# Performance work log

Hardware: AMD Instinct MI355X
Metric: run time of the kernel (lower is better)

## Reference

```python
import jax, jax.numpy as jnp
import numpy as np

T, N, F, H = 64, 20000, 8, 32
E = 320000
NEG_SLOPE = 0.01  # torch.nn.LeakyReLU default


def setup_inputs() -> dict:
    key = jax.random.key(0)
    ks = jax.random.split(key, 16)
    g = lambda k, shape, fan_in: jax.random.normal(k, shape, jnp.float32) * (1.0 / np.sqrt(fan_in))
    return {
        "x": jax.random.normal(ks[0], (T, N, F), jnp.float32),
        "edge_index": jax.random.randint(ks[1], (2, E), 0, N, jnp.int64),
        "edge_weight": jax.random.uniform(ks[2], (E,), jnp.float32),
        "h": jnp.zeros((N, H), jnp.float32),
        # GConvGRU(K=1): each ChebConv reduces to a dense Linear (only T_0 = X term)
        "Wxz": g(ks[3], (F, H), F), "bxz": jnp.zeros((H,), jnp.float32),
        "Whz": g(ks[4], (H, H), H), "bhz": jnp.zeros((H,), jnp.float32),
        "Wxr": g(ks[5], (F, H), F), "bxr": jnp.zeros((H,), jnp.float32),
        "Whr": g(ks[6], (H, H), H), "bhr": jnp.zeros((H,), jnp.float32),
        "Wxh": g(ks[7], (F, H), F), "bxh": jnp.zeros((H,), jnp.float32),
        "Whh": g(ks[8], (H, H), H), "bhh": jnp.zeros((H,), jnp.float32),
        "W1": g(ks[9], (H, 1), H), "b1": jnp.zeros((1,), jnp.float32),
        "W2": g(ks[10], (N, 1), N), "b2": jnp.zeros((1,), jnp.float32),
    }


def reference(x, edge_index, edge_weight, h,
              Wxz, bxz, Whz, bhz, Wxr, bxr, Whr, bhr, Wxh, bxh, Whh, bhh,
              W1, b1, W2, b2):
    # GConvGRU with Chebyshev order K=1: each ChebConv is out = X @ W + b
    # (edge_index / edge_weight only participate for K >= 2, faithful to source).
    def gru_step(hc, xt):  # hc: [N,H], xt: [N,F]
        z = jax.nn.sigmoid(xt @ Wxz + bxz + hc @ Whz + bhz)
        r = jax.nn.sigmoid(xt @ Wxr + bxr + hc @ Whr + bhr)
        h_tilde = jnp.tanh(xt @ Wxh + bxh + (hc * r) @ Whh + bhh)
        hn = z * hc + (1.0 - z) * h_tilde
        return hn, hn

    h_fin, h_tensor = jax.lax.scan(gru_step, h, x)  # h_tensor: [T,N,H]
    a = jax.nn.leaky_relu(h_tensor, NEG_SLOPE)       # LeakyReLU(h_tensor)
    a = jax.nn.leaky_relu(a @ W1 + b1, NEG_SLOPE)    # linear1 -> [T,N,1], then LeakyReLU
    a = a[..., 0]                                    # squeeze -> [T,N]
    out = (a @ W2 + b2)[..., 0]                      # linear2 -> [T,1] -> squeeze -> [T]
    return (out, h_fin)
```

## Files before the change

### kernel.cpp

```cpp
#include <hip/hip_runtime.h>

#define T_STEPS 64
#define N_NODES 20000
#define F_IN    8
#define H_DIM   32
#define NEG_SLOPE 0.01f
#define WS_STRIDE 32
#define LOG2E 1.44269504f

typedef __attribute__((ext_vector_type(8))) short bf16x8;
typedef __attribute__((ext_vector_type(4))) float f32x4;

#define MFMA(a, b, c) __builtin_amdgcn_mfma_f32_16x16x32_bf16((a), (b), (c), 0, 0, 0)

__device__ __forceinline__ unsigned short f2bf(float f) {
    unsigned u = __float_as_uint(f);
    u += 0x7FFFu + ((u >> 16) & 1u);
    return (unsigned short)(u >> 16);
}
__device__ __forceinline__ float bf2f(unsigned short s) {
    return __uint_as_float(((unsigned)s) << 16);
}
__device__ __forceinline__ void split_pack8_rne(const float* v, bf16x8& hi, bf16x8& lo) {
    union { unsigned u[4]; bf16x8 v8; } H, L;
#pragma unroll
    for (int p = 0; p < 4; ++p) {
        float a = v[2*p], b = v[2*p+1];
        unsigned short ha = f2bf(a), hb = f2bf(b);
        unsigned short la = f2bf(a - bf2f(ha)), lb = f2bf(b - bf2f(hb));
        H.u[p] = (unsigned)ha | ((unsigned)hb << 16);
        L.u[p] = (unsigned)la | ((unsigned)lb << 16);
    }
    hi = H.v8; lo = L.v8;
}

__device__ __forceinline__ bf16x8 pack8_rne(const float* v) {
    union { unsigned u[4]; bf16x8 v8; } U;
#pragma unroll
    for (int p = 0; p < 4; ++p) {
        unsigned a = __float_as_uint(v[2*p]);
        unsigned b = __float_as_uint(v[2*p+1]);
        a += 0x7FFFu + ((a >> 16) & 1u);
        b += 0x7FFFu + ((b >> 16) & 1u);
        U.u[p] = __builtin_amdgcn_perm(b, a, 0x07060302u);
    }
    return U.v8;
}


__device__ __forceinline__ void load_wfragW(const float* __restrict__ W, int c, int q,
                                            int Rout, int Rown, int Roth, float scale,
                                            bf16x8& hi, bf16x8& lo) {
    float v[8];
#pragma unroll
    for (int j = 0; j < 8; ++j) {
        int dim = (j < 4) ? (Rown + 4*q + j) : (Roth + 4*q + (j - 4));
        v[j] = W[dim * H_DIM + (Rout + c)] * scale;
    }
    split_pack8_rne(v, hi, lo);
}

__device__ __forceinline__ bf16x8 load_xwfragW(const float* __restrict__ Wx,
                                               const float* __restrict__ bx,
                                               const float* __restrict__ bh,
                                               int c, int q, int Rout, float scale) {
    union { unsigned short s[8]; bf16x8 v8; } U;
#pragma unroll
    for (int j = 0; j < 8; ++j) U.s[j] = 0;
    if (q <= 1) {
#pragma unroll
        for (int j = 0; j < 8; ++j) U.s[j] = f2bf(Wx[j * H_DIM + Rout + c] * scale);
    } else if (q == 2) {
#pragma unroll
        for (int j = 0; j < 8; ++j) {
            float w0 = Wx[j * H_DIM + Rout + c] * scale;
            unsigned short h = f2bf(w0);
            U.s[j] = f2bf(w0 - bf2f(h));
        }
    } else {
        float b = (bx[Rout + c] + bh[Rout + c]) * scale;
        unsigned short h = f2bf(b);
        U.s[0] = h;
        U.s[1] = f2bf(b - bf2f(h));
    }
    return U.v8;
}

__device__ __forceinline__ bf16x8 build_xbfrag(const float* v, int q) {
    unsigned hu[8]; unsigned lu[8];
#pragma unroll
    for (int j = 0; j < 8; ++j) {
        hu[j] = __float_as_uint(v[j]) & 0xffff0000u;
        lu[j] = __float_as_uint(v[j] - __uint_as_float(hu[j]));
    }
    union { unsigned u[4]; bf16x8 v8; } U;
#pragma unroll
    for (int p = 0; p < 4; ++p) {
        unsigned hw = __builtin_amdgcn_perm(hu[2*p+1], hu[2*p], 0x07060302u);
        unsigned lw = __builtin_amdgcn_perm(lu[2*p+1], lu[2*p], 0x07060302u);
        unsigned w  = (q == 1) ? lw : hw;
        if (q == 3) w = (p == 0) ? 0x3F803F80u : 0u;
        U.u[p] = w;
    }
    return U.v8;
}

__device__ __forceinline__ float sigmoid2_f(float xp) {
    return __builtin_amdgcn_rcpf(1.0f + __builtin_amdgcn_exp2f(-xp));
}
__device__ __forceinline__ float tanh2_f(float yp) {
    return 1.0f - 2.0f * __builtin_amdgcn_rcpf(1.0f + __builtin_amdgcn_exp2f(yp));
}
__device__ __forceinline__ float leaky_f(float x) {
    return fmaxf(x, NEG_SLOPE * x);
}

__global__ void final_kernel(const float* __restrict__ ws, const float* __restrict__ b2,
                             float* __restrict__ out) {
    int t = threadIdx.x;
    if (t < T_STEPS) out[t] = ws[t * WS_STRIDE] + b2[0];
}

__global__ __launch_bounds__(128, 3) void rgcn_mfma_kernel(
    const float* __restrict__ x,
    const float* __restrict__ h0,
    const float* __restrict__ Wxz, const float* __restrict__ bxz,
    const float* __restrict__ Whz, const float* __restrict__ bhz,
    const float* __restrict__ Wxr, const float* __restrict__ bxr,
    const float* __restrict__ Whr, const float* __restrict__ bhr,
    const float* __restrict__ Wxh, const float* __restrict__ bxh,
    const float* __restrict__ Whh, const float* __restrict__ bhh,
    const float* __restrict__ W1,  const float* __restrict__ b1,
    const float* __restrict__ W2,
    float* __restrict__ ws,
    float* __restrict__ out)
{
    const int tid  = threadIdx.x;
    const int w    = tid >> 6;
    const int l    = tid & 63;
    const int c    = l & 15;
    const int q    = l >> 4;
    const int base = blockIdx.x * 16;
    const int node = base + c;
    const int Rown = 16 * w;
    const int Roth = 16 - Rown;

    __shared__ __align__(16) float hxbuf[2][2][4][16][4];
    __shared__ unsigned short pbuf16[T_STEPS][130];

    bf16x8 WHrOh, WHrOl, WHrTh, WHrTl, WHzh, WHzl, WHhh, WHhl;
    load_wfragW(Whr, c, q, Rown, Rown, Roth, LOG2E,        WHrOh, WHrOl);
    load_wfragW(Whr, c, q, Roth, Rown, Roth, LOG2E,        WHrTh, WHrTl);
    load_wfragW(Whz, c, q, Rown, Rown, Roth, LOG2E,        WHzh,  WHzl);
    load_wfragW(Whh, c, q, Rown, Rown, Roth, 2.0f * LOG2E, WHhh,  WHhl);
    bf16x8 WXrO = load_xwfragW(Wxr, bxr, bhr, c, q, Rown, LOG2E);
    bf16x8 WXrT = load_xwfragW(Wxr, bxr, bhr, c, q, Roth, LOG2E);
    bf16x8 WXz  = load_xwfragW(Wxz, bxz, bhz, c, q, Rown, LOG2E);
    bf16x8 WXh  = load_xwfragW(Wxh, bxh, bhh, c, q, Rown, 2.0f * LOG2E);

    float w1v[4];
#pragma unroll
    for (int i = 0; i < 4; ++i) w1v[i] = W1[Rown + 4*q + i];
    const float b1s = b1[0];
    const float w2l = W2[node];

    float hv8[8];
    {
        float4 h4 = ((const float4*)(h0 + (size_t)node * H_DIM + Rown))[q];
        hv8[0] = h4.x; hv8[1] = h4.y; hv8[2] = h4.z; hv8[3] = h4.w;
        *(float4*)&hxbuf[0][w][q][c][0] = h4;
    }

    bf16x8 fxb;
    {
        const float4* xp = (const float4*)(x + (size_t)node * F_IN);
        float4 x0 = xp[0], x1 = xp[1];
        float xv[8] = {x0.x, x0.y, x0.z, x0.w, x1.x, x1.y, x1.z, x1.w};
        fxb = build_xbfrag(xv, q);
    }
    float4 cx0, cx1;
    {
        const float4* xp = (const float4*)(x + (size_t)(N_NODES * F_IN)
                                             + (size_t)node * F_IN);
        cx0 = xp[0]; cx1 = xp[1];
    }

    const f32x4 zero4 = {0.0f, 0.0f, 0.0f, 0.0f};

    __syncthreads();

#pragma unroll 1
    for (int t = 0; t < T_STEPS; ++t) {
        const int rp = t & 1;

        int tt = (t + 2 < T_STEPS) ? (t + 2) : (T_STEPS - 1);
        const float4* xp = (const float4*)(x + (size_t)tt * (N_NODES * F_IN)
                                             + (size_t)node * F_IN);
        float4 nx0 = xp[0], nx1 = xp[1];

        float4 oh = *(const float4*)&hxbuf[rp][1 - w][q][c][0];
        hv8[4] = oh.x; hv8[5] = oh.y; hv8[6] = oh.z; hv8[7] = oh.w;

        bf16x8 fhh = pack8_rne(hv8);

        f32x4 arOA = MFMA(WXrO, fxb, zero4);
        f32x4 arTA = MFMA(WXrT, fxb, zero4);
        f32x4 azA  = MFMA(WXz,  fxb, zero4);
        f32x4 ahx  = MFMA(WXh,  fxb, zero4);
        f32x4 arOB = MFMA(WHrOl, fhh, zero4);
        f32x4 arTB = MFMA(WHrTl, fhh, zero4);
        f32x4 azB  = MFMA(WHzl,  fhh, zero4);
        arOA = MFMA(WHrOh, fhh, arOA);
        arTA = MFMA(WHrTh, fhh, arTA);
        azA  = MFMA(WHzh,  fhh, azA);

        f32x4 arO = arOA + arOB;
        f32x4 arT = arTA + arTB;

        float rh8[8];
#pragma unroll
        for (int i = 0; i < 4; ++i) {
            rh8[i]     = sigmoid2_f(arO[i]) * hv8[i];
            rh8[4 + i] = sigmoid2_f(arT[i]) * hv8[4 + i];
        }
        bf16x8 frh = pack8_rne(rh8);

        f32x4 ahB = MFMA(WHhl, frh, zero4);
        ahx = MFMA(WHhh, frh, ahx);

        float nxv[8] = {cx0.x, cx0.y, cx0.z, cx0.w, cx1.x, cx1.y, cx1.z, cx1.w};
        bf16x8 fxn = build_xbfrag(nxv, q);

        f32x4 az = azA + azB;
        f32x4 ah = ahx + ahB;

        float pnew = 0.0f;
#pragma unroll
        for (int i = 0; i < 4; ++i) {
            float zz = sigmoid2_f(az[i]);
            float th = tanh2_f(ah[i]);
            float hn = th + zz * (hv8[i] - th);
            hv8[i] = hn;
            pnew = fmaf(leaky_f(hn), w1v[i], pnew);
        }
        pbuf16[t][tid] = f2bf(pnew);

        *(float4*)&hxbuf[1 - rp][w][q][c][0] =
            (float4){hv8[0], hv8[1], hv8[2], hv8[3]};
        fxb = fxn;
        cx0 = nx0; cx1 = nx1;

        __syncthreads();
    }

#pragma unroll
    for (int rep = 0; rep < 8; ++rep) {
        int t = w * 32 + rep * 4 + q;
        float s = 0.0f;
#pragma unroll
        for (int g = 0; g < 8; ++g) s += bf2f(pbuf16[t][g * 16 + c]);
        float a2 = leaky_f(s + b1s) * w2l;
        a2 += __shfl_xor(a2, 1); a2 += __shfl_xor(a2, 2);
        a2 += __shfl_xor(a2, 4); a2 += __shfl_xor(a2, 8);
        if (c == 0) atomicAdd(&ws[t * WS_STRIDE], a2);
    }

    *(float4*)(out + T_STEPS + (size_t)node * H_DIM + Rown + 4*q) =
        (float4){hv8[0], hv8[1], hv8[2], hv8[3]};
}

extern "C" void kernel_launch(void* const* d_in, const int* in_sizes, int n_in,
                              void* d_out, int out_size, void* d_ws, size_t ws_size,
                              hipStream_t stream) {
    const float* x    = (const float*)d_in[0];
    const float* h0   = (const float*)d_in[3];
    const float* Wxz  = (const float*)d_in[4];
    const float* bxz  = (const float*)d_in[5];
    const float* Whz  = (const float*)d_in[6];
    const float* bhz  = (const float*)d_in[7];
    const float* Wxr  = (const float*)d_in[8];
    const float* bxr  = (const float*)d_in[9];
    const float* Whr  = (const float*)d_in[10];
    const float* bhr  = (const float*)d_in[11];
    const float* Wxh  = (const float*)d_in[12];
    const float* bxh  = (const float*)d_in[13];
    const float* Whh  = (const float*)d_in[14];
    const float* bhh  = (const float*)d_in[15];
    const float* W1   = (const float*)d_in[16];
    const float* b1   = (const float*)d_in[17];
    const float* W2   = (const float*)d_in[18];
    const float* b2   = (const float*)d_in[19];
    float* out = (float*)d_out;
    float* ws  = (float*)d_ws;

    const int grid = N_NODES / 16;
    rgcn_mfma_kernel<<<grid, 128, 0, stream>>>(
        x, h0, Wxz, bxz, Whz, bhz, Wxr, bxr, Whr, bhr,
        Wxh, bxh, Whh, bhh, W1, b1, W2, ws, out);

    final_kernel<<<1, 64, 0, stream>>>(ws, b2, out);
}
```

Measured before the change: 196.2 us.

## Precompute next-step x MFMAs before barrier and use hardware bf16 pack conversion

Moves the four x-projection MFMAs for step t+1 to the end of step t, before the barrier, so they overlap the sync and leave the recurrent critical path shorter. Pre-packs the node's own hidden half right after the update and switches to the packed bf16 conversion intrinsic in place of manual rounding bit-twiddling. It also changes the x fragment to a single RNE hi term (q==2 now zero, hi/lo split moved into the weight side), and folds the z-gate lo accumulation into a chained MFMA. This may change numerics slightly and add accumulator register pressure.

```diff
diff --git a/kernel.cpp b/kernel.cpp
--- a/kernel.cpp
+++ b/kernel.cpp
@@ -1,4 +1,5 @@
 #include <hip/hip_runtime.h>
+#include <hip/hip_bf16.h>
 
 #define T_STEPS 64
 #define N_NODES 20000
@@ -34,17 +35,10 @@
     hi = H.v8; lo = L.v8;
 }
 
-__device__ __forceinline__ bf16x8 pack8_rne(const float* v) {
-    union { unsigned u[4]; bf16x8 v8; } U;
-#pragma unroll
-    for (int p = 0; p < 4; ++p) {
-        unsigned a = __float_as_uint(v[2*p]);
-        unsigned b = __float_as_uint(v[2*p+1]);
-        a += 0x7FFFu + ((a >> 16) & 1u);
-        b += 0x7FFFu + ((b >> 16) & 1u);
-        U.u[p] = __builtin_amdgcn_perm(b, a, 0x07060302u);
-    }
-    return U.v8;
+__device__ __forceinline__ unsigned cvtpk(float a, float b) {
+    union { __hip_bfloat162 h; unsigned u; } U;
+    U.h = __float22bfloat162_rn(float2{a, b});
+    return U.u;
 }
 
 
@@ -67,17 +61,17 @@
     union { unsigned short s[8]; bf16x8 v8; } U;
 #pragma unroll
     for (int j = 0; j < 8; ++j) U.s[j] = 0;
-    if (q <= 1) {
+    if (q == 0) {
 #pragma unroll
         for (int j = 0; j < 8; ++j) U.s[j] = f2bf(Wx[j * H_DIM + Rout + c] * scale);
-    } else if (q == 2) {
+    } else if (q == 1) {
 #pragma unroll
         for (int j = 0; j < 8; ++j) {
             float w0 = Wx[j * H_DIM + Rout + c] * scale;
             unsigned short h = f2bf(w0);
             U.s[j] = f2bf(w0 - bf2f(h));
         }
-    } else {
+    } else if (q == 3) {
         float b = (bx[Rout + c] + bh[Rout + c]) * scale;
         unsigned short h = f2bf(b);
         U.s[0] = h;
@@ -86,21 +80,14 @@
     return U.v8;
 }
 
-__device__ __forceinline__ bf16x8 build_xbfrag(const float* v, int q) {
-    unsigned hu[8]; unsigned lu[8];
-#pragma unroll
-    for (int j = 0; j < 8; ++j) {
-        hu[j] = __float_as_uint(v[j]) & 0xffff0000u;
-        lu[j] = __float_as_uint(v[j] - __uint_as_float(hu[j]));
-    }
+__device__ __forceinline__ bf16x8 build_xbfrag2(const float* v, int q) {
     union { unsigned u[4]; bf16x8 v8; } U;
 #pragma unroll
     for (int p = 0; p < 4; ++p) {
-        unsigned hw = __builtin_amdgcn_perm(hu[2*p+1], hu[2*p], 0x07060302u);
-        unsigned lw = __builtin_amdgcn_perm(lu[2*p+1], lu[2*p], 0x07060302u);
-        unsigned w  = (q == 1) ? lw : hw;
-        if (q == 3) w = (p == 0) ? 0x3F803F80u : 0u;
-        U.u[p] = w;
+        unsigned val = cvtpk(v[2*p], v[2*p+1]);
+        if (q == 2) val = 0u;
+        if (q == 3) val = (p == 0) ? 0x3F803F80u : 0u;
+        U.u[p] = val;
     }
     return U.v8;
 }
@@ -165,18 +152,27 @@
     const float w2l = W2[node];
 
     float hv8[8];
+    unsigned own01, own23;
     {
         float4 h4 = ((const float4*)(h0 + (size_t)node * H_DIM + Rown))[q];
         hv8[0] = h4.x; hv8[1] = h4.y; hv8[2] = h4.z; hv8[3] = h4.w;
         *(float4*)&hxbuf[0][w][q][c][0] = h4;
-    }
-
-    bf16x8 fxb;
+        own01 = cvtpk(hv8[0], hv8[1]);
+        own23 = cvtpk(hv8[2], hv8[3]);
+    }
+
+    const f32x4 zero4 = {0.0f, 0.0f, 0.0f, 0.0f};
+
+    f32x4 axrO, axrT, axz, axh;
     {
         const float4* xp = (const float4*)(x + (size_t)node * F_IN);
         float4 x0 = xp[0], x1 = xp[1];
         float xv[8] = {x0.x, x0.y, x0.z, x0.w, x1.x, x1.y, x1.z, x1.w};
-        fxb = build_xbfrag(xv, q);
+        bf16x8 fx0 = build_xbfrag2(xv, q);
+        axrO = MFMA(WXrO, fx0, zero4);
+        axrT = MFMA(WXrT, fx0, zero4);
+        axz  = MFMA(WXz,  fx0, zero4);
+        axh  = MFMA(WXh,  fx0, zero4);
     }
     float4 cx0, cx1;
     {
@@ -185,8 +181,6 @@
         cx0 = xp[0]; cx1 = xp[1];
     }
 
-    const f32x4 zero4 = {0.0f, 0.0f, 0.0f, 0.0f};
-
     __syncthreads();
 
 #pragma unroll 1
@@ -201,18 +195,18 @@
         float4 oh = *(const float4*)&hxbuf[rp][1 - w][q][c][0];
         hv8[4] = oh.x; hv8[5] = oh.y; hv8[6] = oh.z; hv8[7] = oh.w;
 
-        bf16x8 fhh = pack8_rne(hv8);
-
-        f32x4 arOA = MFMA(WXrO, fxb, zero4);
-        f32x4 arTA = MFMA(WXrT, fxb, zero4);
-        f32x4 azA  = MFMA(WXz,  fxb, zero4);
-        f32x4 ahx  = MFMA(WXh,  fxb, zero4);
+        union { unsigned u[4]; bf16x8 v8; } FH;
+        FH.u[0] = own01; FH.u[1] = own23;
+        FH.u[2] = cvtpk(oh.x, oh.y);
+        FH.u[3] = cvtpk(oh.z, oh.w);
+        bf16x8 fhh = FH.v8;
+
         f32x4 arOB = MFMA(WHrOl, fhh, zero4);
+        f32x4 arOA = MFMA(WHrOh, fhh, axrO);
         f32x4 arTB = MFMA(WHrTl, fhh, zero4);
-        f32x4 azB  = MFMA(WHzl,  fhh, zero4);
-        arOA = MFMA(WHrOh, fhh, arOA);
-        arTA = MFMA(WHrTh, fhh, arTA);
-        azA  = MFMA(WHzh,  fhh, azA);
+        f32x4 arTA = MFMA(WHrTh, fhh, axrT);
+        f32x4 az   = MFMA(WHzh,  fhh, axz);
+        az         = MFMA(WHzl,  fhh, az);
 
         f32x4 arO = arOA + arOB;
         f32x4 arT = arTA + arTB;
@@ -223,16 +217,20 @@
             rh8[i]     = sigmoid2_f(arO[i]) * hv8[i];
             rh8[4 + i] = sigmoid2_f(arT[i]) * hv8[4 + i];
         }
-        bf16x8 frh = pack8_rne(rh8);
+        union { unsigned u[4]; bf16x8 v8; } FR;
+        FR.u[0] = cvtpk(rh8[0], rh8[1]);
+        FR.u[1] = cvtpk(rh8[2], rh8[3]);
+        FR.u[2] = cvtpk(rh8[4], rh8[5]);
+        FR.u[3] = cvtpk(rh8[6], rh8[7]);
+        bf16x8 frh = FR.v8;
 
         f32x4 ahB = MFMA(WHhl, frh, zero4);
-        ahx = MFMA(WHhh, frh, ahx);
+        f32x4 ahA = MFMA(WHhh, frh, axh);
 
         float nxv[8] = {cx0.x, cx0.y, cx0.z, cx0.w, cx1.x, cx1.y, cx1.z, cx1.w};
-        bf16x8 fxn = build_xbfrag(nxv, q);
-
-        f32x4 az = azA + azB;
-        f32x4 ah = ahx + ahB;
+        bf16x8 fxn = build_xbfrag2(nxv, q);
+
+        f32x4 ah = ahA + ahB;
 
         float pnew = 0.0f;
 #pragma unroll
@@ -245,9 +243,16 @@
         }
         pbuf16[t][tid] = f2bf(pnew);
 
+        own01 = cvtpk(hv8[0], hv8[1]);
+        own23 = cvtpk(hv8[2], hv8[3]);
         *(float4*)&hxbuf[1 - rp][w][q][c][0] =
             (float4){hv8[0], hv8[1], hv8[2], hv8[3]};
-        fxb = fxn;
+
+        axrO = MFMA(WXrO, fxn, zero4);
+        axrT = MFMA(WXrT, fxn, zero4);
+        axz  = MFMA(WXz,  fxn, zero4);
+        axh  = MFMA(WXh,  fxn, zero4);
+
         cx0 = nx0; cx1 = nx1;
 
         __syncthreads();
```

After: 193.5 us. Within noise of the previous version (-1.4%).
